# Performance work log

Hardware: AMD Instinct MI355X
Metric: run time of the kernel (lower is better)

Reference implementation:

```python
import jax, jax.numpy as jnp
import numpy as np
from jax import lax

B, N, C = 4, 1024, 384
H, G, K = 6, 2, 10
GD = C // G   # group dim = 192
HD = C // H   # head dim = 64
SCALE = HD ** -0.5
LN_EPS = 1e-5


def _sqdist(a, b):
    # a: [..., M, 3], b: [..., N, 3] -> squared euclid dist [..., M, N]
    return (jnp.sum(a * a, -1)[..., :, None]
            - 2.0 * jnp.einsum('...mc,...nc->...mn', a, b)
            + jnp.sum(b * b, -1)[..., None, :])


def _layernorm(x, g, b):
    mu = jnp.mean(x, -1, keepdims=True)
    var = jnp.mean(jnp.square(x - mu), -1, keepdims=True)
    return (x - mu) * lax.rsqrt(var + LN_EPS) * g + b


def _forward(q, q_pos, Wq, Wk, Wv, Wvoff, W1, b1, ln_g, ln_b, W2, Wproj, bproj):
    # self-attention path: v = q, v_pos = q_pos
    bidx = jnp.arange(B)[:, None, None]
    # KNN over positions: idx [B, N, K]
    d = _sqdist(q_pos, q_pos)
    _, idx = lax.top_k(-d, K)
    qp = q @ Wq                       # [B, N, C]
    v_off = q @ Wvoff                 # [B, N, C]
    local_v = v_off[bidx, idx]        # [B, N, K, C]
    # split channels into groups: 'b n k (g c) -> b g n k c'
    off_local_v = local_v.reshape(B, N, K, G, GD).transpose(0, 3, 1, 2, 4)
    group_q = qp.reshape(B, N, G, GD).transpose(0, 2, 1, 3)      # [B, G, N, GD]
    shift_feat = jnp.concatenate(
        [off_local_v, jnp.broadcast_to(group_q[:, :, :, None, :], (B, G, N, K, GD))], -1)
    h = _layernorm(shift_feat @ W1 + b1, ln_g, ln_b)
    h = jax.nn.gelu(h, approximate=False)
    offset = jnp.tanh(h @ W2)                                    # [B, G, N, K, 3]
    local_v_pos = q_pos[bidx, idx]                               # [B, N, K, 3]
    shift_pos = (local_v_pos[:, None] + offset).reshape(B, G, N * K, 3)
    # three_nn: 3 nearest v_pos points for each shifted point (squared dists, as in CUDA kernel)
    v_pos_g = jnp.broadcast_to(q_pos[:, None], (B, G, N, 3))
    d2 = _sqdist(shift_pos, v_pos_g)                             # [B, G, N*K, N]
    neg_d3, idx3 = lax.top_k(-d2, 3)
    dist3 = -neg_d3                                              # ascending
    rec = 1.0 / (dist3 + 1e-8)
    w = rec / jnp.sum(rec, -1, keepdims=True)                    # [B, G, N*K, 3]
    # three_interpolate on grouped v features
    v_g = q.reshape(B, N, G, GD).transpose(0, 2, 1, 3)           # [B, G, N, GD]
    gathered = v_g[jnp.arange(B)[:, None, None, None],
                   jnp.arange(G)[None, :, None, None], idx3]      # [B, G, N*K, 3, GD]
    interp = jnp.sum(w[..., None] * gathered, 3)                 # [B, G, N*K, GD]
    # '(b g) (n k) c -> b n k (g c)'
    interp = interp.reshape(B, G, N, K, GD).transpose(0, 2, 3, 1, 4).reshape(B, N, K, C)
    # local cross attention: 1 query vs K keys per token per head
    kk = (interp @ Wk).reshape(B, N, K, H, HD)
    vv = (interp @ Wv).reshape(B, N, K, H, HD)
    qh = qp.reshape(B, N, H, HD)
    attn = jnp.einsum('bnhd,bnkhd->bnhk', qh, kk) * SCALE
    attn = jax.nn.softmax(attn, -1)
    out = jnp.einsum('bnhk,bnkhd->bnhd', attn, vv).reshape(B, N, C)
    return out @ Wproj + bproj


def setup_inputs() -> dict:
    key = jax.random.key(0)
    ks = jax.random.split(key, 12)
    s = 0.02
    return {
        'q': jax.random.normal(ks[0], (B, N, C), jnp.float32),
        'q_pos': jax.random.normal(ks[1], (B, N, 3), jnp.float32),
        'Wq': s * jax.random.normal(ks[2], (C, C), jnp.float32),
        'Wk': s * jax.random.normal(ks[3], (C, C), jnp.float32),
        'Wv': s * jax.random.normal(ks[4], (C, C), jnp.float32),
        'Wvoff': s * jax.random.normal(ks[5], (C, C), jnp.float32),
        'W1': s * jax.random.normal(ks[6], (2 * GD, C), jnp.float32),
        'b1': jnp.zeros((C,), jnp.float32),
        'ln_g': jnp.ones((C,), jnp.float32),
        'ln_b': jnp.zeros((C,), jnp.float32),
        'W2': s * jax.random.normal(ks[7], (C, 3), jnp.float32),
        'Wproj': s * jax.random.normal(ks[8], (C, C), jnp.float32),
        'bproj': jnp.zeros((C,), jnp.float32),
    }


def reference(q, q_pos, Wq, Wk, Wv, Wvoff, W1, b1, ln_g, ln_b, W2, Wproj, bproj):
    return _forward(q, q_pos, Wq, Wk, Wv, Wvoff, W1, b1, ln_g, ln_b, W2, Wproj, bproj)
```

## Files before the change

### kernel.cpp

```cpp
#include <hip/hip_runtime.h>
#include <math.h>

constexpr int B_ = 4;
constexpr int N_ = 1024;
constexpr int C_ = 384;
constexpr int G_ = 2;
constexpr int K_ = 10;
constexpr int GD_ = 192;
constexpr int NK_ = N_ * K_;
constexpr int M2_ = B_ * G_ * N_ * K_;
constexpr float SCALE_ = 0.125f;
constexpr float MARGIN_ = 4e-4f;

__device__ __forceinline__ bool lless(double da, int ia, double db, int ib) {
  return (da < db) || (da == db && ia < ib);
}
__device__ __forceinline__ void lmin2(double& rd, int& ri, double ad, int ai,
                                      double bd, int bi) {
  bool t = lless(bd, bi, ad, ai);
  rd = t ? bd : ad; ri = t ? bi : ai;
}
__device__ __forceinline__ void lmax2(double& rd, int& ri, double ad, int ai,
                                      double bd, int bi) {
  bool t = lless(ad, ai, bd, bi);
  rd = t ? bd : ad; ri = t ? bi : ai;
}
__device__ __forceinline__ void pmin2(float& rd, int& ri, float ad, int ai,
                                      float bd, int bi) {
  bool t = bd < ad;
  rd = t ? bd : ad; ri = t ? bi : ai;
}
__device__ __forceinline__ void pmax2(float& rd, int& ri, float ad, int ai,
                                      float bd, int bi) {
  bool t = ad < bd;
  rd = t ? bd : ad; ri = t ? bi : ai;
}

__global__ void k_prep0(const float* __restrict__ q_pos, double* __restrict__ s64,
                        float4* __restrict__ pos4, int* __restrict__ cnt) {
  int i = blockIdx.x * blockDim.x + threadIdx.x;
  if (i == 0) cnt[0] = 0;
  if (i >= B_ * N_) return;
  float x = q_pos[3 * i], y = q_pos[3 * i + 1], z = q_pos[3 * i + 2];
  double v = (double)x * x + (double)y * y + (double)z * z;
  s64[i] = v;
  pos4[i] = make_float4(x, y, z, (float)v);
}

__global__ __launch_bounds__(256) void k_knn10_w(const float* __restrict__ q_pos,
                                                 const double* __restrict__ s,
                                                 int* __restrict__ idx10) {
  int wid = (blockIdx.x * blockDim.x + threadIdx.x) >> 6;
  int lane = threadIdx.x & 63;
  if (wid >= B_ * N_) return;
  int b = wid / N_;
  double px = q_pos[3 * wid], py = q_pos[3 * wid + 1], pz = q_pos[3 * wid + 2];
  double sm = s[wid];
  const float* bp = q_pos + b * N_ * 3;
  const double* bs = s + b * N_;
  double d[K_]; int ix[K_];
  #pragma unroll
  for (int j = 0; j < K_; j++) { d[j] = INFINITY; ix[j] = 0x7fffffff; }
  for (int n0 = 0; n0 < N_; n0 += 64) {
    int n = n0 + lane;
    double dot = px * (double)bp[3 * n] + py * (double)bp[3 * n + 1] +
                 pz * (double)bp[3 * n + 2];
    double v = (sm - 2.0 * dot) + bs[n];
    bool c[K_];
    #pragma unroll
    for (int j = 0; j < K_; j++) c[j] = lless(v, n, d[j], ix[j]);
    #pragma unroll
    for (int j = K_ - 1; j >= 1; j--) {
      d[j]  = c[j] ? (c[j - 1] ? d[j - 1] : v) : d[j];
      ix[j] = c[j] ? (c[j - 1] ? ix[j - 1] : n) : ix[j];
    }
    d[0]  = c[0] ? v : d[0];
    ix[0] = c[0] ? n : ix[0];
  }
  #pragma unroll
  for (int off = 1; off < 64; off <<= 1) {
    double bd[K_]; int bi[K_];
    #pragma unroll
    for (int j = 0; j < K_; j++) {
      bd[j] = __shfl_xor(d[j], off);
      bi[j] = __shfl_xor(ix[j], off);
    }
    double md[K_]; int mi[K_];
    #pragma unroll
    for (int r = 0; r < K_; r++) {
      double m; int mj;
      lmin2(m, mj, d[r], ix[r], bd[r], bi[r]);
      #pragma unroll
      for (int j = 1; j <= r; j++) {
        double t; int ti;
        lmax2(t, ti, d[j - 1], ix[j - 1], bd[r - j], bi[r - j]);
        lmin2(m, mj, m, mj, t, ti);
      }
      md[r] = m; mi[r] = mj;
    }
    #pragma unroll
    for (int j = 0; j < K_; j++) { d[j] = md[j]; ix[j] = mi[j]; }
  }
  if (lane == 0) {
    #pragma unroll
    for (int j = 0; j < K_; j++) idx10[wid * K_ + j] = ix[j];
  }
}

template <int TM>
__global__ __launch_bounds__(384) void k_gemmSA(const float* __restrict__ A,
                                                const float* __restrict__ W,
                                                const float* __restrict__ bias,
                                                float* __restrict__ out, int M) {
  int c = threadIdx.x;
  int r0 = blockIdx.x * TM;
  float acc[TM];
  #pragma unroll
  for (int r = 0; r < TM; r++) acc[r] = 0.f;
  #pragma unroll 4
  for (int j = 0; j < C_; j++) {
    float w = W[j * C_ + c];
    #pragma unroll
    for (int r = 0; r < TM; r++) acc[r] = fmaf(A[(r0 + r) * C_ + j], w, acc[r]);
  }
  float bv = bias ? bias[c] : 0.f;
  #pragma unroll
  for (int r = 0; r < TM; r++) out[(r0 + r) * C_ + c] = acc[r] + bv;
}

__global__ __launch_bounds__(384) void k_prepM(const float* __restrict__ Wvoff,
                                               const float* __restrict__ Wq,
                                               const float* __restrict__ W1,
                                               const float* __restrict__ Wk,
                                               float* __restrict__ M1f,
                                               float* __restrict__ M2f,
                                               float* __restrict__ WkT) {
  int g = blockIdx.x / C_;
  int k = blockIdx.x % C_;
  int c = threadIdx.x;
  if (g == 0) WkT[c * C_ + k] = Wk[k * C_ + c];
  const float* wv = Wvoff + k * C_ + g * GD_;
  const float* wq = Wq + k * C_ + g * GD_;
  double a1 = 0.0, a2 = 0.0;
  for (int d = 0; d < GD_; d++) {
    a1 += (double)wv[d] * (double)W1[d * C_ + c];
    a2 += (double)wq[d] * (double)W1[(GD_ + d) * C_ + c];
  }
  M1f[(g * C_ + k) * C_ + c] = (float)a1;
  M2f[(g * C_ + k) * C_ + c] = (float)a2;
}

template <int TM>
__global__ __launch_bounds__(384) void k_Y32(const float* __restrict__ q,
                                             const float* __restrict__ M1f,
                                             const float* __restrict__ M2f,
                                             float* __restrict__ Y1f,
                                             float* __restrict__ Y2f) {
  int c = threadIdx.x;
  int g = blockIdx.y;
  int r0 = blockIdx.x * TM;
  float a1[TM], a2[TM];
  #pragma unroll
  for (int r = 0; r < TM; r++) { a1[r] = 0.f; a2[r] = 0.f; }
  const float* m1 = M1f + (size_t)(g * C_) * C_ + c;
  const float* m2 = M2f + (size_t)(g * C_) * C_ + c;
  for (int k = 0; k < C_; k++) {
    float v1 = m1[(size_t)k * C_];
    float v2 = m2[(size_t)k * C_];
    #pragma unroll
    for (int r = 0; r < TM; r++) {
      float av = q[(r0 + r) * C_ + k];
      a1[r] = fmaf(av, v1, a1[r]);
      a2[r] = fmaf(av, v2, a2[r]);
    }
  }
  #pragma unroll
  for (int r = 0; r < TM; r++) {
    Y1f[((size_t)(r0 + r) * G_ + g) * C_ + c] = a1[r];
    Y2f[((size_t)(r0 + r) * G_ + g) * C_ + c] = a2[r];
  }
}

__global__ __launch_bounds__(256) void k_mlptop4(const float* __restrict__ Y1f,
                                                 const float* __restrict__ Y2f,
                                                 const int* __restrict__ idx10,
                                                 const float* __restrict__ q_pos,
                                                 const float* __restrict__ b1,
                                                 const float* __restrict__ ln_g,
                                                 const float* __restrict__ ln_b,
                                                 const float* __restrict__ W2,
                                                 const float4* __restrict__ pos4,
                                                 const float* __restrict__ q,
                                                 float* __restrict__ interp,
                                                 int* __restrict__ flags,
                                                 int* __restrict__ cnt) {
  int w_ = threadIdx.x >> 6, l = threadIdx.x & 63;
  int row = blockIdx.x * 4 + w_;
  int k = row % K_; int t = row / K_;
  int n = t % N_; t /= N_;
  int g = t % G_; int b = t / G_;
  int j = idx10[(b * N_ + n) * K_ + k];
  const float* y1 = Y1f + ((size_t)(b * N_ + j) * G_ + g) * C_;
  const float* y2 = Y2f + ((size_t)(b * N_ + n) * G_ + g) * C_;
  float x[6];
  #pragma unroll
  for (int jj = 0; jj < 6; jj++) {
    int col = l + 64 * jj;
    x[jj] = y1[col] + y2[col] + b1[col];
  }
  float sum = ((((x[0] + x[1]) + x[2]) + x[3]) + x[4]) + x[5];
  #pragma unroll
  for (int off = 1; off < 64; off <<= 1) sum += __shfl_xor(sum, off);
  float mu = sum * (1.0f / 384.0f);
  float sq = 0.f;
  #pragma unroll
  for (int jj = 0; jj < 6; jj++) { float dd = x[jj] - mu; sq = fmaf(dd, dd, sq); }
  #pragma unroll
  for (int off = 1; off < 64; off <<= 1) sq += __shfl_xor(sq, off);
  float var = sq * (1.0f / 384.0f);
  float rstd = 1.0f / sqrtf(var + 1e-5f);
  float ge[6];
  #pragma unroll
  for (int jj = 0; jj < 6; jj++) {
    int col = l + 64 * jj;
    float nv = (x[jj] - mu) * rstd * ln_g[col] + ln_b[col];
    ge[jj] = 0.5f * nv * (1.0f + erff(nv * 0.70710678118654752f));
  }
  float o3[3];
  #pragma unroll
  for (int o = 0; o < 3; o++) {
    float p = 0.f;
    #pragma unroll
    for (int jj = 0; jj < 6; jj++) {
      int col = l + 64 * jj;
      p = fmaf(ge[jj], W2[col * 3 + o], p);
    }
    #pragma unroll
    for (int off = 1; off < 64; off <<= 1) p += __shfl_xor(p, off);
    o3[o] = tanhf(p);
  }
  int gi = b * N_ + j;
  float px = q_pos[gi * 3 + 0] + o3[0];
  float py = q_pos[gi * 3 + 1] + o3[1];
  float pz = q_pos[gi * 3 + 2] + o3[2];
  float sp = fmaf(px, px, fmaf(py, py, pz * pz));
  float nx = -2.0f * px, ny = -2.0f * py, nz = -2.0f * pz;
  const float4* p4 = pos4 + b * N_;
  float d0 = INFINITY, d1 = INFINITY, d2 = INFINITY, r4 = INFINITY;
  int i0 = 0x7fffffff, i1 = 0x7fffffff, i2 = 0x7fffffff;
  for (int n0 = 0; n0 < N_; n0 += 64) {
    int nn = n0 + l;
    float4 pv = p4[nn];
    float v = fmaf(nx, pv.x, fmaf(ny, pv.y, fmaf(nz, pv.z, sp + pv.w)));
    bool c0 = v < d0, c1 = v < d1, c2 = v < d2;
    float disp = c2 ? d2 : v;
    r4 = fminf(r4, disp);
    d2 = c2 ? (c1 ? d1 : v) : d2;
    i2 = c2 ? (c1 ? i1 : nn) : i2;
    d1 = c1 ? (c0 ? d0 : v) : d1;
    i1 = c1 ? (c0 ? i0 : nn) : i1;
    d0 = c0 ? v : d0;
    i0 = c0 ? nn : i0;
  }
  #pragma unroll
  for (int off = 1; off < 64; off <<= 1) {
    float e0 = __shfl_xor(d0, off), e1 = __shfl_xor(d1, off), e2 = __shfl_xor(d2, off);
    float er = __shfl_xor(r4, off);
    int j0 = __shfl_xor(i0, off), j1 = __shfl_xor(i1, off), j2 = __shfl_xor(i2, off);
    float va = fmaxf(d0, e2), vb = fmaxf(d1, e1), vc = fmaxf(d2, e0);
    float r4n = fminf(fminf(r4, er), fminf(fminf(va, vb), vc));
    float m0d, t1d, u1d, m1d, t2a, t2b, u2d, w2d, m2d;
    int m0i, t1i, u1i, m1i, t2ai, t2bi, u2i, w2i, m2i;
    pmin2(m0d, m0i, d0, i0, e0, j0);
    pmax2(t1d, t1i, d0, i0, e0, j0);
    pmin2(u1d, u1i, d1, i1, e1, j1);
    pmin2(m1d, m1i, u1d, u1i, t1d, t1i);
    pmax2(t2a, t2ai, d1, i1, e0, j0);
    pmax2(t2b, t2bi, d0, i0, e1, j1);
    pmin2(u2d, u2i, d2, i2, e2, j2);
    pmin2(w2d, w2i, t2a, t2ai, t2b, t2bi);
    pmin2(m2d, m2i, u2d, u2i, w2d, w2i);
    d0 = m0d; i0 = m0i; d1 = m1d; i1 = m1i; d2 = m2d; i2 = m2i; r4 = r4n;
  }
  if (r4 - d2 < MARGIN_) {
    if (l == 0) {
      int pos = atomicAdd(cnt, 1);
      flags[pos] = row;
    }
    return;
  }
  float r0 = 1.0f / (d0 + 1e-8f);
  float r1 = 1.0f / (d1 + 1e-8f);
  float r2 = 1.0f / (d2 + 1e-8f);
  float rs = (r0 + r1) + r2;
  float w0 = r0 / rs, w1 = r1 / rs, w2 = r2 / rs;
  const float* qb = q + (size_t)b * N_ * C_ + g * GD_;
  const float* p0 = qb + (size_t)i0 * C_;
  const float* p1 = qb + (size_t)i1 * C_;
  const float* p2 = qb + (size_t)i2 * C_;
  float* op = interp + (((size_t)(b * N_ + n) * K_ + k) * C_) + g * GD_;
  #pragma unroll
  for (int cc0 = 0; cc0 < GD_; cc0 += 64) {
    int cc = cc0 + l;
    op[cc] = (w0 * p0[cc] + w1 * p1[cc]) + w2 * p2[cc];
  }
}

__global__ __launch_bounds__(256) void k_fix(const int* __restrict__ cnt,
                                             const int* __restrict__ flags,
                                             const float* __restrict__ q,
                                             const float* __restrict__ Wvoff,
                                             const float* __restrict__ Wq,
                                             const float* __restrict__ W1,
                                             const int* __restrict__ idx10,
                                             const float* __restrict__ q_pos,
                                             const double* __restrict__ s64,
                                             const float* __restrict__ b1,
                                             const float* __restrict__ ln_g,
                                             const float* __restrict__ ln_b,
                                             const float* __restrict__ W2,
                                             float* __restrict__ interp) {
  __shared__ double vbuf[4][2][GD_];
  int w_ = threadIdx.x >> 6;
  int gwid = blockIdx.x * 4 + w_;
  int lane = threadIdx.x & 63;
  int nwaves = gridDim.x * 4;
  int total = cnt[0];
  for (int i = gwid; i < total; i += nwaves) {
    int wid = __builtin_amdgcn_readfirstlane(flags[i]);
    int m = wid % NK_; int t = wid / NK_;
    int g = t % G_; int b = t / G_;
    int n_ = m / K_, k_ = m % K_;
    int j = __builtin_amdgcn_readfirstlane(idx10[(b * N_ + n_) * K_ + k_]);
    const float* qj = q + (size_t)(b * N_ + j) * C_;
    const float* qn = q + (size_t)(b * N_ + n_) * C_;
    const float* wvo = Wvoff + g * GD_;
    const float* wqg = Wq + g * GD_;
    double a0 = 0.0, a1 = 0.0, a2 = 0.0, b0 = 0.0, b1a = 0.0, b2 = 0.0;
    for (int tt = 0; tt < C_; tt++) {
      double qjt = (double)qj[tt];
      double qnt = (double)qn[tt];
      const float* r1 = wvo + (size_t)tt * C_;
      const float* r2 = wqg + (size_t)tt * C_;
      a0 += qjt * (double)r1[lane];
      a1 += qjt * (double)r1[lane + 64];
      a2 += qjt * (double)r1[lane + 128];
      b0 += qnt * (double)r2[lane];
      b1a += qnt * (double)r2[lane + 64];
      b2 += qnt * (double)r2[lane + 128];
    }
    vbuf[w_][0][lane] = a0; vbuf[w_][0][lane + 64] = a1; vbuf[w_][0][lane + 128] = a2;
    vbuf[w_][1][lane] = b0; vbuf[w_][1][lane + 64] = b1a; vbuf[w_][1][lane + 128] = b2;
    double x[6];
    #pragma unroll
    for (int jj = 0; jj < 6; jj++) x[jj] = 0.0;
    for (int d = 0; d < GD_; d++) {
      double v1d = vbuf[w_][0][d];
      double v2d = vbuf[w_][1][d];
      const float* w1t = W1 + (size_t)d * C_;
      const float* w1b = W1 + (size_t)(GD_ + d) * C_;
      #pragma unroll
      for (int jj = 0; jj < 6; jj++) {
        int col = lane + 64 * jj;
        x[jj] += v1d * (double)w1t[col] + v2d * (double)w1b[col];
      }
    }
    #pragma unroll
    for (int jj = 0; jj < 6; jj++) x[jj] += (double)b1[lane + 64 * jj];
    double sum = ((((x[0] + x[1]) + x[2]) + x[3]) + x[4]) + x[5];
    #pragma unroll
    for (int off = 1; off < 64; off <<= 1) sum += __shfl_xor(sum, off);
    double mu = sum / 384.0;
    double sq = 0.0;
    #pragma unroll
    for (int jj = 0; jj < 6; jj++) { double dd = x[jj] - mu; sq += dd * dd; }
    #pragma unroll
    for (int off = 1; off < 64; off <<= 1) sq += __shfl_xor(sq, off);
    double var = sq / 384.0;
    double rstd = 1.0 / sqrt(var + 1e-5);
    double ge[6];
    #pragma unroll
    for (int jj = 0; jj < 6; jj++) {
      int col = lane + 64 * jj;
      double nv = (x[jj] - mu) * rstd * (double)ln_g[col] + (double)ln_b[col];
      ge[jj] = 0.5 * nv * (1.0 + erf(nv * 0.70710678118654752440));
    }
    double o3[3];
    #pragma unroll
    for (int o = 0; o < 3; o++) {
      double p = 0.0;
      #pragma unroll
      for (int jj = 0; jj < 6; jj++) {
        int col = lane + 64 * jj;
        p += ge[jj] * (double)W2[col * 3 + o];
      }
      #pragma unroll
      for (int off = 1; off < 64; off <<= 1) p += __shfl_xor(p, off);
      o3[o] = tanh(p);
    }
    int gi = b * N_ + j;
    double px = (double)q_pos[gi * 3 + 0] + o3[0];
    double py = (double)q_pos[gi * 3 + 1] + o3[1];
    double pz = (double)q_pos[gi * 3 + 2] + o3[2];
    double sp = px * px + py * py + pz * pz;
    const float* bp = q_pos + b * N_ * 3;
    const double* bs = s64 + b * N_;
    double d0 = INFINITY, d1 = INFINITY, d2 = INFINITY;
    int i0 = 0x7fffffff, i1 = 0x7fffffff, i2 = 0x7fffffff;
    for (int n = lane; n < N_; n += 64) {
      double dot = px * (double)bp[3 * n] + py * (double)bp[3 * n + 1] +
                   pz * (double)bp[3 * n + 2];
      double dd = (sp - 2.0 * dot) + bs[n];
      bool c0 = lless(dd, n, d0, i0);
      bool c1 = lless(dd, n, d1, i1);
      bool c2 = lless(dd, n, d2, i2);
      double nd2 = c2 ? (c1 ? d1 : dd) : d2; int ni2 = c2 ? (c1 ? i1 : n) : i2;
      double nd1 = c1 ? (c0 ? d0 : dd) : d1; int ni1 = c1 ? (c0 ? i0 : n) : i1;
      double nd0 = c0 ? dd : d0;             int ni0 = c0 ? n : i0;
      d0 = nd0; d1 = nd1; d2 = nd2; i0 = ni0; i1 = ni1; i2 = ni2;
    }
    #pragma unroll
    for (int off = 1; off < 64; off <<= 1) {
      double e0 = __shfl_xor(d0, off), e1 = __shfl_xor(d1, off), e2 = __shfl_xor(d2, off);
      int j0 = __shfl_xor(i0, off), j1 = __shfl_xor(i1, off), j2 = __shfl_xor(i2, off);
      double mnd, mxd, p1d, q1d, q2d, q3d, q4d, t1d, t2d;
      int mni, mxi, p1i, q1i, q2i, q3i, q4i, t1i, t2i;
      lmin2(mnd, mni, d0, i0, e0, j0);
      lmax2(mxd, mxi, d0, i0, e0, j0);
      lmin2(p1d, p1i, d1, i1, e1, j1);
      lmin2(t1d, t1i, p1d, p1i, mxd, mxi);
      lmax2(q1d, q1i, d1, i1, e0, j0);
      lmax2(q2d, q2i, d0, i0, e1, j1);
      lmin2(q3d, q3i, q1d, q1i, q2d, q2i);
      lmin2(q4d, q4i, d2, i2, e2, j2);
      lmin2(t2d, t2i, q3d, q3i, q4d, q4i);
      d0 = mnd; i0 = mni; d1 = t1d; i1 = t1i; d2 = t2d; i2 = t2i;
    }
    double r0 = 1.0 / (d0 + 1e-8);
    double r1 = 1.0 / (d1 + 1e-8);
    double r2 = 1.0 / (d2 + 1e-8);
    double rs = (r0 + r1) + r2;
    float w0 = (float)(r0 / rs), w1 = (float)(r1 / rs), w2 = (float)(r2 / rs);
    const float* qb = q + (size_t)b * N_ * C_ + g * GD_;
    const float* p0 = qb + (size_t)i0 * C_;
    const float* p1 = qb + (size_t)i1 * C_;
    const float* p2 = qb + (size_t)i2 * C_;
    float* op = interp + (((size_t)(b * N_ + n_) * K_ + k_) * C_) + g * GD_;
    #pragma unroll
    for (int cc0 = 0; cc0 < GD_; cc0 += 64) {
      int cc = cc0 + lane;
      op[cc] = (w0 * p0[cc] + w1 * p1[cc]) + w2 * p2[cc];
    }
  }
}

template <int TM>
__global__ __launch_bounds__(384) void k_U(const float* __restrict__ qp,
                                           const float* __restrict__ WkT,
                                           float* __restrict__ U) {
  int c = threadIdx.x;
  int r0 = blockIdx.x * TM;
  for (int h = 0; h < 6; h++) {
    float acc[TM];
    #pragma unroll
    for (int r = 0; r < TM; r++) acc[r] = 0.f;
    #pragma unroll 4
    for (int dd = 0; dd < 64; dd++) {
      float w = WkT[(h * 64 + dd) * C_ + c];
      #pragma unroll
      for (int r = 0; r < TM; r++)
        acc[r] = fmaf(qp[(r0 + r) * C_ + h * 64 + dd], w, acc[r]);
    }
    #pragma unroll
    for (int r = 0; r < TM; r++) U[((size_t)(r0 + r) * 6 + h) * C_ + c] = acc[r];
  }
}

__global__ __launch_bounds__(256) void k_attn2(const float* __restrict__ interp,
                                               float* __restrict__ Umix) {
  int wid = blockIdx.x * 4 + (threadIdx.x >> 6);
  int lane = threadIdx.x & 63;
  int bn = wid / 6;
  float* urow = Umix + (size_t)wid * C_;
  float u[6];
  #pragma unroll
  for (int j = 0; j < 6; j++) u[j] = urow[lane + 64 * j];
  float ipv[K_][6];
  float logit[K_];
  #pragma unroll
  for (int k = 0; k < K_; k++) {
    const float* ip = interp + ((size_t)bn * K_ + k) * C_;
    float p = 0.f;
    #pragma unroll
    for (int j = 0; j < 6; j++) {
      ipv[k][j] = ip[lane + 64 * j];
      p = fmaf(ipv[k][j], u[j], p);
    }
    #pragma unroll
    for (int off = 1; off < 64; off <<= 1) p += __shfl_xor(p, off);
    logit[k] = p * SCALE_;
  }
  float mx = logit[0];
  #pragma unroll
  for (int k = 1; k < K_; k++) mx = fmaxf(mx, logit[k]);
  float e[K_], se = 0.f;
  #pragma unroll
  for (int k = 0; k < K_; k++) { e[k] = expf(logit[k] - mx); se += e[k]; }
  float inv = 1.0f / se;
  #pragma unroll
  for (int k = 0; k < K_; k++) e[k] *= inv;
  #pragma unroll
  for (int j = 0; j < 6; j++) {
    float mv = 0.f;
    #pragma unroll
    for (int k = 0; k < K_; k++) mv = fmaf(e[k], ipv[k][j], mv);
    urow[lane + 64 * j] = mv;
  }
}

template <int TM>
__global__ __launch_bounds__(384) void k_out(const float* __restrict__ mix,
                                             const float* __restrict__ Wv,
                                             float* __restrict__ attn_out) {
  int c = threadIdx.x;
  int h = __builtin_amdgcn_readfirstlane(threadIdx.x) >> 6;
  int r0 = blockIdx.x * TM;
  float acc[TM];
  #pragma unroll
  for (int r = 0; r < TM; r++) acc[r] = 0.f;
  #pragma unroll 4
  for (int ci = 0; ci < C_; ci++) {
    float w = Wv[ci * C_ + c];
    #pragma unroll
    for (int r = 0; r < TM; r++)
      acc[r] = fmaf(mix[((size_t)(r0 + r) * 6 + h) * C_ + ci], w, acc[r]);
  }
  #pragma unroll
  for (int r = 0; r < TM; r++) attn_out[(size_t)(r0 + r) * C_ + c] = acc[r];
}

extern "C" void kernel_launch(void* const* d_in, const int* in_sizes, int n_in,
                              void* d_out, int out_size, void* d_ws, size_t ws_size,
                              hipStream_t stream) {
  const float* q     = (const float*)d_in[0];
  const float* q_pos = (const float*)d_in[1];
  const float* Wq    = (const float*)d_in[2];
  const float* Wk    = (const float*)d_in[3];
  const float* Wv    = (const float*)d_in[4];
  const float* Wvoff = (const float*)d_in[5];
  const float* W1    = (const float*)d_in[6];
  const float* b1    = (const float*)d_in[7];
  const float* ln_g  = (const float*)d_in[8];
  const float* ln_b  = (const float*)d_in[9];
  const float* W2    = (const float*)d_in[10];
  const float* Wproj = (const float*)d_in[11];
  const float* bproj = (const float*)d_in[12];
  float* out = (float*)d_out;

  char* ws = (char*)d_ws;
  char* U0 = ws; ws += 38 * 1024 * 1024;
  float*  Y1f    = (float*)(U0);
  float*  Y2f    = (float*)(U0 + 12582912);
  float*  M1f    = (float*)(U0 + 25165824);
  float*  M2f    = (float*)(U0 + 26345472);
  int*    idx10  = (int*)  (U0 + 28508160);
  int*    flags  = (int*)  (U0 + 28672000);
  float4* pos4   = (float4*)(U0 + 28999680);
  int*    cnt    = (int*)  (U0 + 29065216);
  float*  Umix   = (float*)U0;
  double* s64    = (double*)ws; ws += (size_t)B_ * N_ * 8;
  float*  qp32   = (float*)ws;  ws += (size_t)B_ * N_ * C_ * 4;
  float*  interp = (float*)ws;  ws += (size_t)B_ * N_ * K_ * C_ * 4;
  float*  WkT    = (float*)ws;  ws += (size_t)C_ * C_ * 4;
  float*  attn_out = qp32;

  k_prep0<<<(B_ * N_ + 255) / 256, 256, 0, stream>>>(q_pos, s64, pos4, cnt);
  k_knn10_w<<<B_ * N_ / 4, 256, 0, stream>>>(q_pos, s64, idx10);
  k_gemmSA<8><<<B_ * N_ / 8, 384, 0, stream>>>(q, Wq, nullptr, qp32, B_ * N_);
  k_prepM<<<G_ * C_, 384, 0, stream>>>(Wvoff, Wq, W1, Wk, M1f, M2f, WkT);
  k_Y32<8><<<dim3(B_ * N_ / 8, G_), 384, 0, stream>>>(q, M1f, M2f, Y1f, Y2f);
  k_mlptop4<<<M2_ / 4, 256, 0, stream>>>(Y1f, Y2f, idx10, q_pos, b1, ln_g, ln_b,
                                         W2, pos4, q, interp, flags, cnt);
  k_fix<<<512, 256, 0, stream>>>(cnt, flags, q, Wvoff, Wq, W1, idx10, q_pos, s64,
                                 b1, ln_g, ln_b, W2, interp);
  k_U<8><<<B_ * N_ / 8, 384, 0, stream>>>(qp32, WkT, Umix);
  k_attn2<<<B_ * N_ * 6 / 4, 256, 0, stream>>>(interp, Umix);
  k_out<8><<<B_ * N_ / 8, 384, 0, stream>>>(Umix, Wv, attn_out);
  k_gemmSA<8><<<B_ * N_ / 8, 384, 0, stream>>>(attn_out, Wproj, bproj, out, B_ * N_);
}
```

Baseline: 646.0 us.

## Merge independent kernels into shared launches and fuse output projections

Independent stages now share a launch, with block ranges dispatching to different work: weight prep with position prep, KNN with the Wq GEMM, and the fix-up pass with the U GEMM. Attention is reworked to handle several heads per block. The Wv and Wproj GEMMs are fused through shared memory so the intermediate never goes to global memory, tanh/exp use fast approximations, and the workspace is re-laid out. The aim is fewer launches, overlap of independent work, and less global traffic, at the cost of heterogeneous blocks that can load-balance poorly and slightly lower-precision math.

```diff
diff --git a/kernel.cpp b/kernel.cpp
--- a/kernel.cpp
+++ b/kernel.cpp
@@ -12,6 +12,13 @@
 constexpr float SCALE_ = 0.125f;
 constexpr float MARGIN_ = 4e-4f;
 
+constexpr int L1_PREPM_ = G_ * C_;
+constexpr int L1_GRID_ = L1_PREPM_ + 11;
+constexpr int L2_KNN_ = 683;
+constexpr int L2_GRID_ = L2_KNN_ + 512;
+constexpr int L4_FIX_ = 256;
+constexpr int L4_GRID_ = L4_FIX_ + 512;
+
 __device__ __forceinline__ bool lless(double da, int ia, double db, int ib) {
   return (da < db) || (da == db && ia < ib);
 }
@@ -35,122 +42,127 @@
   bool t = ad < bd;
   rd = t ? bd : ad; ri = t ? bi : ai;
 }
-
-__global__ void k_prep0(const float* __restrict__ q_pos, double* __restrict__ s64,
-                        float4* __restrict__ pos4, int* __restrict__ cnt) {
-  int i = blockIdx.x * blockDim.x + threadIdx.x;
-  if (i == 0) cnt[0] = 0;
-  if (i >= B_ * N_) return;
-  float x = q_pos[3 * i], y = q_pos[3 * i + 1], z = q_pos[3 * i + 2];
-  double v = (double)x * x + (double)y * y + (double)z * z;
-  s64[i] = v;
-  pos4[i] = make_float4(x, y, z, (float)v);
-}
-
-__global__ __launch_bounds__(256) void k_knn10_w(const float* __restrict__ q_pos,
-                                                 const double* __restrict__ s,
-                                                 int* __restrict__ idx10) {
-  int wid = (blockIdx.x * blockDim.x + threadIdx.x) >> 6;
-  int lane = threadIdx.x & 63;
-  if (wid >= B_ * N_) return;
-  int b = wid / N_;
-  double px = q_pos[3 * wid], py = q_pos[3 * wid + 1], pz = q_pos[3 * wid + 2];
-  double sm = s[wid];
-  const float* bp = q_pos + b * N_ * 3;
-  const double* bs = s + b * N_;
-  double d[K_]; int ix[K_];
-  #pragma unroll
-  for (int j = 0; j < K_; j++) { d[j] = INFINITY; ix[j] = 0x7fffffff; }
-  for (int n0 = 0; n0 < N_; n0 += 64) {
-    int n = n0 + lane;
-    double dot = px * (double)bp[3 * n] + py * (double)bp[3 * n + 1] +
-                 pz * (double)bp[3 * n + 2];
-    double v = (sm - 2.0 * dot) + bs[n];
-    bool c[K_];
-    #pragma unroll
-    for (int j = 0; j < K_; j++) c[j] = lless(v, n, d[j], ix[j]);
-    #pragma unroll
-    for (int j = K_ - 1; j >= 1; j--) {
-      d[j]  = c[j] ? (c[j - 1] ? d[j - 1] : v) : d[j];
-      ix[j] = c[j] ? (c[j - 1] ? ix[j - 1] : n) : ix[j];
-    }
-    d[0]  = c[0] ? v : d[0];
-    ix[0] = c[0] ? n : ix[0];
-  }
-  #pragma unroll
-  for (int off = 1; off < 64; off <<= 1) {
-    double bd[K_]; int bi[K_];
-    #pragma unroll
-    for (int j = 0; j < K_; j++) {
-      bd[j] = __shfl_xor(d[j], off);
-      bi[j] = __shfl_xor(ix[j], off);
-    }
-    double md[K_]; int mi[K_];
-    #pragma unroll
-    for (int r = 0; r < K_; r++) {
-      double m; int mj;
-      lmin2(m, mj, d[r], ix[r], bd[r], bi[r]);
-      #pragma unroll
-      for (int j = 1; j <= r; j++) {
-        double t; int ti;
-        lmax2(t, ti, d[j - 1], ix[j - 1], bd[r - j], bi[r - j]);
-        lmin2(m, mj, m, mj, t, ti);
-      }
-      md[r] = m; mi[r] = mj;
-    }
-    #pragma unroll
-    for (int j = 0; j < K_; j++) { d[j] = md[j]; ix[j] = mi[j]; }
-  }
-  if (lane == 0) {
-    #pragma unroll
-    for (int j = 0; j < K_; j++) idx10[wid * K_ + j] = ix[j];
-  }
-}
-
-template <int TM>
-__global__ __launch_bounds__(384) void k_gemmSA(const float* __restrict__ A,
-                                                const float* __restrict__ W,
-                                                const float* __restrict__ bias,
-                                                float* __restrict__ out, int M) {
-  int c = threadIdx.x;
-  int r0 = blockIdx.x * TM;
-  float acc[TM];
-  #pragma unroll
-  for (int r = 0; r < TM; r++) acc[r] = 0.f;
-  #pragma unroll 4
-  for (int j = 0; j < C_; j++) {
-    float w = W[j * C_ + c];
-    #pragma unroll
-    for (int r = 0; r < TM; r++) acc[r] = fmaf(A[(r0 + r) * C_ + j], w, acc[r]);
-  }
-  float bv = bias ? bias[c] : 0.f;
-  #pragma unroll
-  for (int r = 0; r < TM; r++) out[(r0 + r) * C_ + c] = acc[r] + bv;
-}
-
-__global__ __launch_bounds__(384) void k_prepM(const float* __restrict__ Wvoff,
-                                               const float* __restrict__ Wq,
-                                               const float* __restrict__ W1,
-                                               const float* __restrict__ Wk,
-                                               float* __restrict__ M1f,
-                                               float* __restrict__ M2f,
-                                               float* __restrict__ WkT) {
-  int g = blockIdx.x / C_;
-  int k = blockIdx.x % C_;
-  int c = threadIdx.x;
-  if (g == 0) WkT[c * C_ + k] = Wk[k * C_ + c];
-  const float* wv = Wvoff + k * C_ + g * GD_;
-  const float* wq = Wq + k * C_ + g * GD_;
-  double a1 = 0.0, a2 = 0.0;
-  for (int d = 0; d < GD_; d++) {
-    a1 += (double)wv[d] * (double)W1[d * C_ + c];
-    a2 += (double)wq[d] * (double)W1[(GD_ + d) * C_ + c];
-  }
-  M1f[(g * C_ + k) * C_ + c] = (float)a1;
-  M2f[(g * C_ + k) * C_ + c] = (float)a2;
-}
-
-template <int TM>
+__device__ __forceinline__ float ftanh(float p) {
+  float pc = fminf(fmaxf(p, -15.f), 15.f);
+  float e = __expf(2.f * pc);
+  return (e - 1.f) * __builtin_amdgcn_rcpf(e + 1.f);
+}
+
+__global__ __launch_bounds__(384) void k_L1(const float* __restrict__ Wvoff,
+                                            const float* __restrict__ Wq,
+                                            const float* __restrict__ W1,
+                                            const float* __restrict__ Wk,
+                                            const float* __restrict__ q_pos,
+                                            float* __restrict__ M1f,
+                                            float* __restrict__ M2f,
+                                            float* __restrict__ WkT,
+                                            double* __restrict__ s64,
+                                            float4* __restrict__ pos4,
+                                            int* __restrict__ cnt) {
+  if (blockIdx.x < L1_PREPM_) {
+    int g = blockIdx.x / C_;
+    int k = blockIdx.x % C_;
+    int c = threadIdx.x;
+    if (g == 0) WkT[c * C_ + k] = Wk[k * C_ + c];
+    const float* wv = Wvoff + k * C_ + g * GD_;
+    const float* wq = Wq + k * C_ + g * GD_;
+    double a1 = 0.0, a2 = 0.0;
+    for (int d = 0; d < GD_; d++) {
+      a1 += (double)wv[d] * (double)W1[d * C_ + c];
+      a2 += (double)wq[d] * (double)W1[(GD_ + d) * C_ + c];
+    }
+    M1f[(g * C_ + k) * C_ + c] = (float)a1;
+    M2f[(g * C_ + k) * C_ + c] = (float)a2;
+  } else {
+    int i = (blockIdx.x - L1_PREPM_) * 384 + threadIdx.x;
+    if (i == 0) cnt[0] = 0;
+    if (i >= B_ * N_) return;
+    float x = q_pos[3 * i], y = q_pos[3 * i + 1], z = q_pos[3 * i + 2];
+    double v = (double)x * x + (double)y * y + (double)z * z;
+    s64[i] = v;
+    pos4[i] = make_float4(x, y, z, (float)v);
+  }
+}
+
+__global__ __launch_bounds__(384) void k_L2a(const float* __restrict__ q_pos,
+                                             const double* __restrict__ s,
+                                             int* __restrict__ idx10,
+                                             const float* __restrict__ q,
+                                             const float* __restrict__ Wq,
+                                             float* __restrict__ qp) {
+  if (blockIdx.x < L2_KNN_) {
+    int wid = blockIdx.x * 6 + (threadIdx.x >> 6);
+    int lane = threadIdx.x & 63;
+    if (wid >= B_ * N_) return;
+    int b = wid / N_;
+    double px = q_pos[3 * wid], py = q_pos[3 * wid + 1], pz = q_pos[3 * wid + 2];
+    double sm = s[wid];
+    const float* bp = q_pos + b * N_ * 3;
+    const double* bs = s + b * N_;
+    double d[K_]; int ix[K_];
+    #pragma unroll
+    for (int j = 0; j < K_; j++) { d[j] = INFINITY; ix[j] = 0x7fffffff; }
+    for (int n0 = 0; n0 < N_; n0 += 64) {
+      int n = n0 + lane;
+      double dot = px * (double)bp[3 * n] + py * (double)bp[3 * n + 1] +
+                   pz * (double)bp[3 * n + 2];
+      double v = (sm - 2.0 * dot) + bs[n];
+      bool c[K_];
+      #pragma unroll
+      for (int j = 0; j < K_; j++) c[j] = lless(v, n, d[j], ix[j]);
+      #pragma unroll
+      for (int j = K_ - 1; j >= 1; j--) {
+        d[j]  = c[j] ? (c[j - 1] ? d[j - 1] : v) : d[j];
+        ix[j] = c[j] ? (c[j - 1] ? ix[j - 1] : n) : ix[j];
+      }
+      d[0]  = c[0] ? v : d[0];
+      ix[0] = c[0] ? n : ix[0];
+    }
+    #pragma unroll
+    for (int off = 1; off < 64; off <<= 1) {
+      double bd[K_]; int bi[K_];
+      #pragma unroll
+      for (int j = 0; j < K_; j++) {
+        bd[j] = __shfl_xor(d[j], off);
+        bi[j] = __shfl_xor(ix[j], off);
+      }
+      double md[K_]; int mi[K_];
+      #pragma unroll
+      for (int r = 0; r < K_; r++) {
+        double m; int mj;
+        lmin2(m, mj, d[r], ix[r], bd[r], bi[r]);
+        #pragma unroll
+        for (int j = 1; j <= r; j++) {
+          double t; int ti;
+          lmax2(t, ti, d[j - 1], ix[j - 1], bd[r - j], bi[r - j]);
+          lmin2(m, mj, m, mj, t, ti);
+        }
+        md[r] = m; mi[r] = mj;
+      }
+      #pragma unroll
+      for (int j = 0; j < K_; j++) { d[j] = md[j]; ix[j] = mi[j]; }
+    }
+    if (lane == 0) {
+      #pragma unroll
+      for (int j = 0; j < K_; j++) idx10[wid * K_ + j] = ix[j];
+    }
+  } else {
+    int c = threadIdx.x;
+    int r0 = (blockIdx.x - L2_KNN_) * 8;
+    float acc[8];
+    #pragma unroll
+    for (int r = 0; r < 8; r++) acc[r] = 0.f;
+    #pragma unroll 4
+    for (int j = 0; j < C_; j++) {
+      float w = Wq[j * C_ + c];
+      #pragma unroll
+      for (int r = 0; r < 8; r++) acc[r] = fmaf(q[(r0 + r) * C_ + j], w, acc[r]);
+    }
+    #pragma unroll
+    for (int r = 0; r < 8; r++) qp[(r0 + r) * C_ + c] = acc[r];
+  }
+}
+
 __global__ __launch_bounds__(384) void k_Y32(const float* __restrict__ q,
                                              const float* __restrict__ M1f,
                                              const float* __restrict__ M2f,
@@ -158,30 +170,30 @@
                                              float* __restrict__ Y2f) {
   int c = threadIdx.x;
   int g = blockIdx.y;
-  int r0 = blockIdx.x * TM;
-  float a1[TM], a2[TM];
-  #pragma unroll
-  for (int r = 0; r < TM; r++) { a1[r] = 0.f; a2[r] = 0.f; }
+  int r0 = blockIdx.x * 8;
+  float a1[8], a2[8];
+  #pragma unroll
+  for (int r = 0; r < 8; r++) { a1[r] = 0.f; a2[r] = 0.f; }
   const float* m1 = M1f + (size_t)(g * C_) * C_ + c;
   const float* m2 = M2f + (size_t)(g * C_) * C_ + c;
   for (int k = 0; k < C_; k++) {
     float v1 = m1[(size_t)k * C_];
     float v2 = m2[(size_t)k * C_];
     #pragma unroll
-    for (int r = 0; r < TM; r++) {
+    for (int r = 0; r < 8; r++) {
       float av = q[(r0 + r) * C_ + k];
       a1[r] = fmaf(av, v1, a1[r]);
       a2[r] = fmaf(av, v2, a2[r]);
     }
   }
   #pragma unroll
-  for (int r = 0; r < TM; r++) {
+  for (int r = 0; r < 8; r++) {
     Y1f[((size_t)(r0 + r) * G_ + g) * C_ + c] = a1[r];
     Y2f[((size_t)(r0 + r) * G_ + g) * C_ + c] = a2[r];
   }
 }
 
-__global__ __launch_bounds__(256) void k_mlptop4(const float* __restrict__ Y1f,
+__global__ __launch_bounds__(384) void k_mlptop4(const float* __restrict__ Y1f,
                                                  const float* __restrict__ Y2f,
                                                  const int* __restrict__ idx10,
                                                  const float* __restrict__ q_pos,
@@ -195,7 +207,8 @@
                                                  int* __restrict__ flags,
                                                  int* __restrict__ cnt) {
   int w_ = threadIdx.x >> 6, l = threadIdx.x & 63;
-  int row = blockIdx.x * 4 + w_;
+  int row = blockIdx.x * 6 + w_;
+  if (row >= M2_) return;
   int k = row % K_; int t = row / K_;
   int n = t % N_; t /= N_;
   int g = t % G_; int b = t / G_;
@@ -237,7 +250,7 @@
     }
     #pragma unroll
     for (int off = 1; off < 64; off <<= 1) p += __shfl_xor(p, off);
-    o3[o] = tanhf(p);
+    o3[o] = ftanh(p);
   }
   int gi = b * N_ + j;
   float px = q_pos[gi * 3 + 0] + o3[0];
@@ -306,237 +319,256 @@
   }
 }
 
-__global__ __launch_bounds__(256) void k_fix(const int* __restrict__ cnt,
-                                             const int* __restrict__ flags,
-                                             const float* __restrict__ q,
-                                             const float* __restrict__ Wvoff,
-                                             const float* __restrict__ Wq,
-                                             const float* __restrict__ W1,
-                                             const int* __restrict__ idx10,
-                                             const float* __restrict__ q_pos,
-                                             const double* __restrict__ s64,
-                                             const float* __restrict__ b1,
-                                             const float* __restrict__ ln_g,
-                                             const float* __restrict__ ln_b,
-                                             const float* __restrict__ W2,
-                                             float* __restrict__ interp) {
-  __shared__ double vbuf[4][2][GD_];
-  int w_ = threadIdx.x >> 6;
-  int gwid = blockIdx.x * 4 + w_;
-  int lane = threadIdx.x & 63;
-  int nwaves = gridDim.x * 4;
-  int total = cnt[0];
-  for (int i = gwid; i < total; i += nwaves) {
-    int wid = __builtin_amdgcn_readfirstlane(flags[i]);
-    int m = wid % NK_; int t = wid / NK_;
-    int g = t % G_; int b = t / G_;
-    int n_ = m / K_, k_ = m % K_;
-    int j = __builtin_amdgcn_readfirstlane(idx10[(b * N_ + n_) * K_ + k_]);
-    const float* qj = q + (size_t)(b * N_ + j) * C_;
-    const float* qn = q + (size_t)(b * N_ + n_) * C_;
-    const float* wvo = Wvoff + g * GD_;
-    const float* wqg = Wq + g * GD_;
-    double a0 = 0.0, a1 = 0.0, a2 = 0.0, b0 = 0.0, b1a = 0.0, b2 = 0.0;
-    for (int tt = 0; tt < C_; tt++) {
-      double qjt = (double)qj[tt];
-      double qnt = (double)qn[tt];
-      const float* r1 = wvo + (size_t)tt * C_;
-      const float* r2 = wqg + (size_t)tt * C_;
-      a0 += qjt * (double)r1[lane];
-      a1 += qjt * (double)r1[lane + 64];
-      a2 += qjt * (double)r1[lane + 128];
-      b0 += qnt * (double)r2[lane];
-      b1a += qnt * (double)r2[lane + 64];
-      b2 += qnt * (double)r2[lane + 128];
-    }
-    vbuf[w_][0][lane] = a0; vbuf[w_][0][lane + 64] = a1; vbuf[w_][0][lane + 128] = a2;
-    vbuf[w_][1][lane] = b0; vbuf[w_][1][lane + 64] = b1a; vbuf[w_][1][lane + 128] = b2;
-    double x[6];
-    #pragma unroll
-    for (int jj = 0; jj < 6; jj++) x[jj] = 0.0;
-    for (int d = 0; d < GD_; d++) {
-      double v1d = vbuf[w_][0][d];
-      double v2d = vbuf[w_][1][d];
-      const float* w1t = W1 + (size_t)d * C_;
-      const float* w1b = W1 + (size_t)(GD_ + d) * C_;
+__global__ __launch_bounds__(384) void k_L4(const int* __restrict__ cnt,
+                                            const int* __restrict__ flags,
+                                            const float* __restrict__ q,
+                                            const float* __restrict__ Wvoff,
+                                            const float* __restrict__ Wq,
+                                            const float* __restrict__ W1,
+                                            const int* __restrict__ idx10,
+                                            const float* __restrict__ q_pos,
+                                            const double* __restrict__ s64,
+                                            const float* __restrict__ b1,
+                                            const float* __restrict__ ln_g,
+                                            const float* __restrict__ ln_b,
+                                            const float* __restrict__ W2,
+                                            float* __restrict__ interp,
+                                            const float* __restrict__ qp,
+                                            const float* __restrict__ WkT,
+                                            float* __restrict__ U) {
+  __shared__ double vbuf[6][2][GD_];
+  if (blockIdx.x < L4_FIX_) {
+    int w_ = threadIdx.x >> 6;
+    int gwid = blockIdx.x * 6 + w_;
+    int lane = threadIdx.x & 63;
+    int nwaves = L4_FIX_ * 6;
+    int total = cnt[0];
+    for (int i = gwid; i < total; i += nwaves) {
+      int wid = __builtin_amdgcn_readfirstlane(flags[i]);
+      int m = wid % NK_; int t = wid / NK_;
+      int g = t % G_; int b = t / G_;
+      int n_ = m / K_, k_ = m % K_;
+      int j = __builtin_amdgcn_readfirstlane(idx10[(b * N_ + n_) * K_ + k_]);
+      const float* qj = q + (size_t)(b * N_ + j) * C_;
+      const float* qn = q + (size_t)(b * N_ + n_) * C_;
+      const float* wvo = Wvoff + g * GD_;
+      const float* wqg = Wq + g * GD_;
+      double a0 = 0.0, a1 = 0.0, a2 = 0.0, b0 = 0.0, b1a = 0.0, b2 = 0.0;
+      for (int tt = 0; tt < C_; tt++) {
+        double qjt = (double)qj[tt];
+        double qnt = (double)qn[tt];
+        const float* r1 = wvo + (size_t)tt * C_;
+        const float* r2 = wqg + (size_t)tt * C_;
+        a0 += qjt * (double)r1[lane];
+        a1 += qjt * (double)r1[lane + 64];
+        a2 += qjt * (double)r1[lane + 128];
+        b0 += qnt * (double)r2[lane];
+        b1a += qnt * (double)r2[lane + 64];
+        b2 += qnt * (double)r2[lane + 128];
+      }
+      vbuf[w_][0][lane] = a0; vbuf[w_][0][lane + 64] = a1; vbuf[w_][0][lane + 128] = a2;
+      vbuf[w_][1][lane] = b0; vbuf[w_][1][lane + 64] = b1a; vbuf[w_][1][lane + 128] = b2;
+      double x[6];
+      #pragma unroll
+      for (int jj = 0; jj < 6; jj++) x[jj] = 0.0;
+      for (int d = 0; d < GD_; d++) {
+        double v1d = vbuf[w_][0][d];
+        double v2d = vbuf[w_][1][d];
+        const float* w1t = W1 + (size_t)d * C_;
+        const float* w1b = W1 + (size_t)(GD_ + d) * C_;
+        #pragma unroll
+        for (int jj = 0; jj < 6; jj++) {
+          int col = lane + 64 * jj;
+          x[jj] += v1d * (double)w1t[col] + v2d * (double)w1b[col];
+        }
+      }
+      #pragma unroll
+      for (int jj = 0; jj < 6; jj++) x[jj] += (double)b1[lane + 64 * jj];
+      double sum = ((((x[0] + x[1]) + x[2]) + x[3]) + x[4]) + x[5];
+      #pragma unroll
+      for (int off = 1; off < 64; off <<= 1) sum += __shfl_xor(sum, off);
+      double mu = sum / 384.0;
+      double sq = 0.0;
+      #pragma unroll
+      for (int jj = 0; jj < 6; jj++) { double dd = x[jj] - mu; sq += dd * dd; }
+      #pragma unroll
+      for (int off = 1; off < 64; off <<= 1) sq += __shfl_xor(sq, off);
+      double var = sq / 384.0;
+      double rstd = 1.0 / sqrt(var + 1e-5);
+      double ge[6];
       #pragma unroll
       for (int jj = 0; jj < 6; jj++) {
         int col = lane + 64 * jj;
-        x[jj] += v1d * (double)w1t[col] + v2d * (double)w1b[col];
-      }
-    }
-    #pragma unroll
-    for (int jj = 0; jj < 6; jj++) x[jj] += (double)b1[lane + 64 * jj];
-    double sum = ((((x[0] + x[1]) + x[2]) + x[3]) + x[4]) + x[5];
-    #pragma unroll
-    for (int off = 1; off < 64; off <<= 1) sum += __shfl_xor(sum, off);
-    double mu = sum / 384.0;
-    double sq = 0.0;
-    #pragma unroll
-    for (int jj = 0; jj < 6; jj++) { double dd = x[jj] - mu; sq += dd * dd; }
-    #pragma unroll
-    for (int off = 1; off < 64; off <<= 1) sq += __shfl_xor(sq, off);
-    double var = sq / 384.0;
-    double rstd = 1.0 / sqrt(var + 1e-5);
-    double ge[6];
-    #pragma unroll
-    for (int jj = 0; jj < 6; jj++) {
-      int col = lane + 64 * jj;
-      double nv = (x[jj] - mu) * rstd * (double)ln_g[col] + (double)ln_b[col];
-      ge[jj] = 0.5 * nv * (1.0 + erf(nv * 0.70710678118654752440));
-    }
-    double o3[3];
-    #pragma unroll
-    for (int o = 0; o < 3; o++) {
-      double p = 0.0;
-      #pragma unroll
-      for (int jj = 0; jj < 6; jj++) {
-        int col = lane + 64 * jj;
-        p += ge[jj] * (double)W2[col * 3 + o];
-      }
+        double nv = (x[jj] - mu) * rstd * (double)ln_g[col] + (double)ln_b[col];
+        ge[jj] = 0.5 * nv * (1.0 + erf(nv * 0.70710678118654752440));
+      }
+      double o3[3];
+      #pragma unroll
+      for (int o = 0; o < 3; o++) {
+        double p = 0.0;
+        #pragma unroll
+        for (int jj = 0; jj < 6; jj++) {
+          int col = lane + 64 * jj;
+          p += ge[jj] * (double)W2[col * 3 + o];
+        }
+        #pragma unroll
+        for (int off = 1; off < 64; off <<= 1) p += __shfl_xor(p, off);
+        o3[o] = tanh(p);
+      }
+      int gi = b * N_ + j;
+      double px = (double)q_pos[gi * 3 + 0] + o3[0];
+      double py = (double)q_pos[gi * 3 + 1] + o3[1];
+      double pz = (double)q_pos[gi * 3 + 2] + o3[2];
+      double sp = px * px + py * py + pz * pz;
+      const float* bp = q_pos + b * N_ * 3;
+      const double* bs = s64 + b * N_;
+      double d0 = INFINITY, d1 = INFINITY, d2 = INFINITY;
+      int i0 = 0x7fffffff, i1 = 0x7fffffff, i2 = 0x7fffffff;
+      for (int n = lane; n < N_; n += 64) {
+        double dot = px * (double)bp[3 * n] + py * (double)bp[3 * n + 1] +
+                     pz * (double)bp[3 * n + 2];
+        double dd = (sp - 2.0 * dot) + bs[n];
+        bool c0 = lless(dd, n, d0, i0);
+        bool c1 = lless(dd, n, d1, i1);
+        bool c2 = lless(dd, n, d2, i2);
+        double nd2 = c2 ? (c1 ? d1 : dd) : d2; int ni2 = c2 ? (c1 ? i1 : n) : i2;
+        double nd1 = c1 ? (c0 ? d0 : dd) : d1; int ni1 = c1 ? (c0 ? i0 : n) : i1;
+        double nd0 = c0 ? dd : d0;             int ni0 = c0 ? n : i0;
+        d0 = nd0; d1 = nd1; d2 = nd2; i0 = ni0; i1 = ni1; i2 = ni2;
+      }
+      #pragma unroll
+      for (int off = 1; off < 64; off <<= 1) {
+        double e0 = __shfl_xor(d0, off), e1 = __shfl_xor(d1, off), e2 = __shfl_xor(d2, off);
+        int j0 = __shfl_xor(i0, off), j1 = __shfl_xor(i1, off), j2 = __shfl_xor(i2, off);
+        double mnd, mxd, p1d, q1d, q2d, q3d, q4d, t1d, t2d;
+        int mni, mxi, p1i, q1i, q2i, q3i, q4i, t1i, t2i;
+        lmin2(mnd, mni, d0, i0, e0, j0);
+        lmax2(mxd, mxi, d0, i0, e0, j0);
+        lmin2(p1d, p1i, d1, i1, e1, j1);
+        lmin2(t1d, t1i, p1d, p1i, mxd, mxi);
+        lmax2(q1d, q1i, d1, i1, e0, j0);
+        lmax2(q2d, q2i, d0, i0, e1, j1);
+        lmin2(q3d, q3i, q1d, q1i, q2d, q2i);
+        lmin2(q4d, q4i, d2, i2, e2, j2);
+        lmin2(t2d, t2i, q3d, q3i, q4d, q4i);
+        d0 = mnd; i0 = mni; d1 = t1d; i1 = t1i; d2 = t2d; i2 = t2i;
+      }
+      double r0 = 1.0 / (d0 + 1e-8);
+      double r1 = 1.0 / (d1 + 1e-8);
+      double r2 = 1.0 / (d2 + 1e-8);
+      double rs = (r0 + r1) + r2;
+      float w0 = (float)(r0 / rs), w1 = (float)(r1 / rs), w2 = (float)(r2 / rs);
+      const float* qb = q + (size_t)b * N_ * C_ + g * GD_;
+      const float* p0 = qb + (size_t)i0 * C_;
+      const float* p1 = qb + (size_t)i1 * C_;
+      const float* p2 = qb + (size_t)i2 * C_;
+      float* op = interp + (((size_t)(b * N_ + n_) * K_ + k_) * C_) + g * GD_;
+      #pragma unroll
+      for (int cc0 = 0; cc0 < GD_; cc0 += 64) {
+        int cc = cc0 + lane;
+        op[cc] = (w0 * p0[cc] + w1 * p1[cc]) + w2 * p2[cc];
+      }
+    }
+  } else {
+    int c = threadIdx.x;
+    int r0 = (blockIdx.x - L4_FIX_) * 8;
+    for (int h = 0; h < 6; h++) {
+      float acc[8];
+      #pragma unroll
+      for (int r = 0; r < 8; r++) acc[r] = 0.f;
+      #pragma unroll 4
+      for (int dd = 0; dd < 64; dd++) {
+        float w = WkT[(h * 64 + dd) * C_ + c];
+        #pragma unroll
+        for (int r = 0; r < 8; r++)
+          acc[r] = fmaf(qp[(r0 + r) * C_ + h * 64 + dd], w, acc[r]);
+      }
+      #pragma unroll
+      for (int r = 0; r < 8; r++) U[((size_t)(r0 + r) * 6 + h) * C_ + c] = acc[r];
+    }
+  }
+}
+
+__global__ __launch_bounds__(384) void k_attn2(const float* __restrict__ interp,
+                                               float* __restrict__ Umix) {
+  int bn = blockIdx.x * 6 + (threadIdx.x >> 6);
+  int lane = threadIdx.x & 63;
+  if (bn >= B_ * N_) return;
+  float ipv[K_][6];
+  const float* ip0 = interp + (size_t)bn * K_ * C_;
+  #pragma unroll
+  for (int k = 0; k < K_; k++) {
+    #pragma unroll
+    for (int j = 0; j < 6; j++) ipv[k][j] = ip0[k * C_ + lane + 64 * j];
+  }
+  float* ubase = Umix + (size_t)bn * 6 * C_;
+  for (int h = 0; h < 6; h++) {
+    float u[6];
+    #pragma unroll
+    for (int j = 0; j < 6; j++) u[j] = ubase[h * C_ + lane + 64 * j];
+    float logit[K_];
+    #pragma unroll
+    for (int k = 0; k < K_; k++) {
+      float p = 0.f;
+      #pragma unroll
+      for (int j = 0; j < 6; j++) p = fmaf(ipv[k][j], u[j], p);
       #pragma unroll
       for (int off = 1; off < 64; off <<= 1) p += __shfl_xor(p, off);
-      o3[o] = tanh(p);
-    }
-    int gi = b * N_ + j;
-    double px = (double)q_pos[gi * 3 + 0] + o3[0];
-    double py = (double)q_pos[gi * 3 + 1] + o3[1];
-    double pz = (double)q_pos[gi * 3 + 2] + o3[2];
-    double sp = px * px + py * py + pz * pz;
-    const float* bp = q_pos + b * N_ * 3;
-    const double* bs = s64 + b * N_;
-    double d0 = INFINITY, d1 = INFINITY, d2 = INFINITY;
-    int i0 = 0x7fffffff, i1 = 0x7fffffff, i2 = 0x7fffffff;
-    for (int n = lane; n < N_; n += 64) {
-      double dot = px * (double)bp[3 * n] + py * (double)bp[3 * n + 1] +
-                   pz * (double)bp[3 * n + 2];
-      double dd = (sp - 2.0 * dot) + bs[n];
-      bool c0 = lless(dd, n, d0, i0);
-      bool c1 = lless(dd, n, d1, i1);
-      bool c2 = lless(dd, n, d2, i2);
-      double nd2 = c2 ? (c1 ? d1 : dd) : d2; int ni2 = c2 ? (c1 ? i1 : n) : i2;
-      double nd1 = c1 ? (c0 ? d0 : dd) : d1; int ni1 = c1 ? (c0 ? i0 : n) : i1;
-      double nd0 = c0 ? dd : d0;             int ni0 = c0 ? n : i0;
-      d0 = nd0; d1 = nd1; d2 = nd2; i0 = ni0; i1 = ni1; i2 = ni2;
-    }
-    #pragma unroll
-    for (int off = 1; off < 64; off <<= 1) {
-      double e0 = __shfl_xor(d0, off), e1 = __shfl_xor(d1, off), e2 = __shfl_xor(d2, off);
-      int j0 = __shfl_xor(i0, off), j1 = __shfl_xor(i1, off), j2 = __shfl_xor(i2, off);
-      double mnd, mxd, p1d, q1d, q2d, q3d, q4d, t1d, t2d;
-      int mni, mxi, p1i, q1i, q2i, q3i, q4i, t1i, t2i;
-      lmin2(mnd, mni, d0, i0, e0, j0);
-      lmax2(mxd, mxi, d0, i0, e0, j0);
-      lmin2(p1d, p1i, d1, i1, e1, j1);
-      lmin2(t1d, t1i, p1d, p1i, mxd, mxi);
-      lmax2(q1d, q1i, d1, i1, e0, j0);
-      lmax2(q2d, q2i, d0, i0, e1, j1);
-      lmin2(q3d, q3i, q1d, q1i, q2d, q2i);
-      lmin2(q4d, q4i, d2, i2, e2, j2);
-      lmin2(t2d, t2i, q3d, q3i, q4d, q4i);
-      d0 = mnd; i0 = mni; d1 = t1d; i1 = t1i; d2 = t2d; i2 = t2i;
-    }
-    double r0 = 1.0 / (d0 + 1e-8);
-    double r1 = 1.0 / (d1 + 1e-8);
-    double r2 = 1.0 / (d2 + 1e-8);
-    double rs = (r0 + r1) + r2;
-    float w0 = (float)(r0 / rs), w1 = (float)(r1 / rs), w2 = (float)(r2 / rs);
-    const float* qb = q + (size_t)b * N_ * C_ + g * GD_;
-    const float* p0 = qb + (size_t)i0 * C_;
-    const float* p1 = qb + (size_t)i1 * C_;
-    const float* p2 = qb + (size_t)i2 * C_;
-    float* op = interp + (((size_t)(b * N_ + n_) * K_ + k_) * C_) + g * GD_;
-    #pragma unroll
-    for (int cc0 = 0; cc0 < GD_; cc0 += 64) {
-      int cc = cc0 + lane;
-      op[cc] = (w0 * p0[cc] + w1 * p1[cc]) + w2 * p2[cc];
-    }
-  }
-}
-
-template <int TM>
-__global__ __launch_bounds__(384) void k_U(const float* __restrict__ qp,
-                                           const float* __restrict__ WkT,
-                                           float* __restrict__ U) {
-  int c = threadIdx.x;
-  int r0 = blockIdx.x * TM;
-  for (int h = 0; h < 6; h++) {
-    float acc[TM];
-    #pragma unroll
-    for (int r = 0; r < TM; r++) acc[r] = 0.f;
-    #pragma unroll 4
-    for (int dd = 0; dd < 64; dd++) {
-      float w = WkT[(h * 64 + dd) * C_ + c];
-      #pragma unroll
-      for (int r = 0; r < TM; r++)
-        acc[r] = fmaf(qp[(r0 + r) * C_ + h * 64 + dd], w, acc[r]);
-    }
-    #pragma unroll
-    for (int r = 0; r < TM; r++) U[((size_t)(r0 + r) * 6 + h) * C_ + c] = acc[r];
-  }
-}
-
-__global__ __launch_bounds__(256) void k_attn2(const float* __restrict__ interp,
-                                               float* __restrict__ Umix) {
-  int wid = blockIdx.x * 4 + (threadIdx.x >> 6);
-  int lane = threadIdx.x & 63;
-  int bn = wid / 6;
-  float* urow = Umix + (size_t)wid * C_;
-  float u[6];
-  #pragma unroll
-  for (int j = 0; j < 6; j++) u[j] = urow[lane + 64 * j];
-  float ipv[K_][6];
-  float logit[K_];
-  #pragma unroll
-  for (int k = 0; k < K_; k++) {
-    const float* ip = interp + ((size_t)bn * K_ + k) * C_;
-    float p = 0.f;
+      logit[k] = p * SCALE_;
+    }
+    float mx = logit[0];
+    #pragma unroll
+    for (int k = 1; k < K_; k++) mx = fmaxf(mx, logit[k]);
+    float e[K_], se = 0.f;
+    #pragma unroll
+    for (int k = 0; k < K_; k++) { e[k] = __expf(logit[k] - mx); se += e[k]; }
+    float inv = 1.0f / se;
+    #pragma unroll
+    for (int k = 0; k < K_; k++) e[k] *= inv;
     #pragma unroll
     for (int j = 0; j < 6; j++) {
-      ipv[k][j] = ip[lane + 64 * j];
-      p = fmaf(ipv[k][j], u[j], p);
-    }
-    #pragma unroll
-    for (int off = 1; off < 64; off <<= 1) p += __shfl_xor(p, off);
-    logit[k] = p * SCALE_;
-  }
-  float mx = logit[0];
-  #pragma unroll
-  for (int k = 1; k < K_; k++) mx = fmaxf(mx, logit[k]);
-  float e[K_], se = 0.f;
-  #pragma unroll
-  for (int k = 0; k < K_; k++) { e[k] = expf(logit[k] - mx); se += e[k]; }
-  float inv = 1.0f / se;
-  #pragma unroll
-  for (int k = 0; k < K_; k++) e[k] *= inv;
-  #pragma unroll
-  for (int j = 0; j < 6; j++) {
-    float mv = 0.f;
-    #pragma unroll
-    for (int k = 0; k < K_; k++) mv = fmaf(e[k], ipv[k][j], mv);
-    urow[lane + 64 * j] = mv;
-  }
-}
-
-template <int TM>
-__global__ __launch_bounds__(384) void k_out(const float* __restrict__ mix,
-                                             const float* __restrict__ Wv,
-                                             float* __restrict__ attn_out) {
+      float mv = 0.f;
+      #pragma unroll
+      for (int k = 0; k < K_; k++) mv = fmaf(e[k], ipv[k][j], mv);
+      ubase[h * C_ + lane + 64 * j] = mv;
+    }
+  }
+}
+
+__global__ __launch_bounds__(384) void k_outproj(const float* __restrict__ mix,
+                                                 const float* __restrict__ Wv,
+                                                 const float* __restrict__ Wproj,
+                                                 const float* __restrict__ bproj,
+                                                 float* __restrict__ out) {
+  __shared__ float ao[8][C_];
   int c = threadIdx.x;
   int h = __builtin_amdgcn_readfirstlane(threadIdx.x) >> 6;
-  int r0 = blockIdx.x * TM;
-  float acc[TM];
-  #pragma unroll
-  for (int r = 0; r < TM; r++) acc[r] = 0.f;
+  int r0 = blockIdx.x * 8;
+  float acc[8];
+  #pragma unroll
+  for (int r = 0; r < 8; r++) acc[r] = 0.f;
   #pragma unroll 4
   for (int ci = 0; ci < C_; ci++) {
     float w = Wv[ci * C_ + c];
     #pragma unroll
-    for (int r = 0; r < TM; r++)
+    for (int r = 0; r < 8; r++)
       acc[r] = fmaf(mix[((size_t)(r0 + r) * 6 + h) * C_ + ci], w, acc[r]);
   }
   #pragma unroll
-  for (int r = 0; r < TM; r++) attn_out[(size_t)(r0 + r) * C_ + c] = acc[r];
+  for (int r = 0; r < 8; r++) ao[r][c] = acc[r];
+  __syncthreads();
+  float a2[8];
+  #pragma unroll
+  for (int r = 0; r < 8; r++) a2[r] = 0.f;
+  #pragma unroll 4
+  for (int ci = 0; ci < C_; ci++) {
+    float w = Wproj[ci * C_ + c];
+    #pragma unroll
+    for (int r = 0; r < 8; r++) a2[r] = fmaf(ao[r][ci], w, a2[r]);
+  }
+  float bv = bproj[c];
+  #pragma unroll
+  for (int r = 0; r < 8; r++) out[(size_t)(r0 + r) * C_ + c] = a2[r] + bv;
 }
 
 extern "C" void kernel_launch(void* const* d_in, const int* in_sizes, int n_in,
@@ -563,28 +595,26 @@
   float*  Y2f    = (float*)(U0 + 12582912);
   float*  M1f    = (float*)(U0 + 25165824);
   float*  M2f    = (float*)(U0 + 26345472);
-  int*    idx10  = (int*)  (U0 + 28508160);
-  int*    flags  = (int*)  (U0 + 28672000);
-  float4* pos4   = (float4*)(U0 + 28999680);
-  int*    cnt    = (int*)  (U0 + 29065216);
   float*  Umix   = (float*)U0;
   double* s64    = (double*)ws; ws += (size_t)B_ * N_ * 8;
   float*  qp32   = (float*)ws;  ws += (size_t)B_ * N_ * C_ * 4;
   float*  interp = (float*)ws;  ws += (size_t)B_ * N_ * K_ * C_ * 4;
   float*  WkT    = (float*)ws;  ws += (size_t)C_ * C_ * 4;
-  float*  attn_out = qp32;
-
-  k_prep0<<<(B_ * N_ + 255) / 256, 256, 0, stream>>>(q_pos, s64, pos4, cnt);
-  k_knn10_w<<<B_ * N_ / 4, 256, 0, stream>>>(q_pos, s64, idx10);
-  k_gemmSA<8><<<B_ * N_ / 8, 384, 0, stream>>>(q, Wq, nullptr, qp32, B_ * N_);
-  k_prepM<<<G_ * C_, 384, 0, stream>>>(Wvoff, Wq, W1, Wk, M1f, M2f, WkT);
-  k_Y32<8><<<dim3(B_ * N_ / 8, G_), 384, 0, stream>>>(q, M1f, M2f, Y1f, Y2f);
-  k_mlptop4<<<M2_ / 4, 256, 0, stream>>>(Y1f, Y2f, idx10, q_pos, b1, ln_g, ln_b,
-                                         W2, pos4, q, interp, flags, cnt);
-  k_fix<<<512, 256, 0, stream>>>(cnt, flags, q, Wvoff, Wq, W1, idx10, q_pos, s64,
-                                 b1, ln_g, ln_b, W2, interp);
-  k_U<8><<<B_ * N_ / 8, 384, 0, stream>>>(qp32, WkT, Umix);
-  k_attn2<<<B_ * N_ * 6 / 4, 256, 0, stream>>>(interp, Umix);
-  k_out<8><<<B_ * N_ / 8, 384, 0, stream>>>(Umix, Wv, attn_out);
-  k_gemmSA<8><<<B_ * N_ / 8, 384, 0, stream>>>(attn_out, Wproj, bproj, out, B_ * N_);
-}
+  int*    idx10  = (int*)ws;    ws += (size_t)B_ * N_ * K_ * 4;
+  int*    flags  = (int*)ws;    ws += (size_t)M2_ * 4;
+  float4* pos4   = (float4*)ws; ws += (size_t)B_ * N_ * 16;
+  int*    cnt    = (int*)ws;    ws += 256;
+
+  k_L1<<<L1_GRID_, 384, 0, stream>>>(Wvoff, Wq, W1, Wk, q_pos, M1f, M2f, WkT,
+                                     s64, pos4, cnt);
+  k_L2a<<<L2_GRID_, 384, 0, stream>>>(q_pos, s64, idx10, q, Wq, qp32);
+  k_Y32<<<dim3(B_ * N_ / 8, G_), 384, 0, stream>>>(q, M1f, M2f, Y1f, Y2f);
+  k_mlptop4<<<(M2_ + 5) / 6, 384, 0, stream>>>(Y1f, Y2f, idx10, q_pos, b1, ln_g,
+                                               ln_b, W2, pos4, q, interp, flags,
+                                               cnt);
+  k_L4<<<L4_GRID_, 384, 0, stream>>>(cnt, flags, q, Wvoff, Wq, W1, idx10, q_pos,
+                                     s64, b1, ln_g, ln_b, W2, interp, qp32, WkT,
+                                     Umix);
+  k_attn2<<<(B_ * N_ + 5) / 6, 384, 0, stream>>>(interp, Umix);
+  k_outproj<<<B_ * N_ / 8, 384, 0, stream>>>(Umix, Wv, Wproj, bproj, out);
+}
```

New measurement: 1.413 ms. 2.19x slower.
